# Performance work log

Hardware: AMD Instinct MI355X
Metric: run time of the kernel (lower is better)

The kernel has to match this reference:

```python
import jax, jax.numpy as jnp
import numpy as np

H = W = 2048
TANH_C = 1.1486328125  # probability-correction constant from the model
DEG2RAD = np.float32(np.pi / 180.0)

# Fire-spread direction angle (degrees, East=0, counterclockwise) from the
# neighbor at 3x3 window position (r, c) toward the center cell.
DIR_DEG = jnp.array([[315., 270., 225.],
                     [  0.,   0., 180.],
                     [ 45.,  90., 135.]], dtype=jnp.float32)
CENTER_MASK = jnp.ones((3, 3), jnp.float32).at[1, 1].set(0.0)  # exclude self


def _neighborhood(x):
    """x: [H,W] -> [H,W,3,3] with [i,j,r,c] = x[i+r-1, j+c-1], zero padded."""
    xp = jnp.pad(x, 1)
    return jnp.stack(
        [jnp.stack([xp[r:r + H, c:c + W] for c in range(3)], axis=-1)
         for r in range(3)], axis=-2)


def setup_inputs() -> dict:
    key = jax.random.key(0)
    ks = jax.random.split(key, 8)
    p_veg = jax.random.uniform(ks[0], (H, W), jnp.float32)
    p_den = jax.random.uniform(ks[1], (H, W), jnp.float32)
    wind_velocity = jax.random.uniform(ks[2], (H, W), jnp.float32) * 10.0
    wind_towards_direction = jax.random.uniform(ks[3], (H, W), jnp.float32) * 360.0
    slope = (jax.random.uniform(ks[4], (H, W, 3, 3), jnp.float32) - 0.5) * 60.0
    burning = jax.random.uniform(ks[5], (H, W)) < 0.01  # sparse initial ignition
    burned = jnp.zeros((H, W), dtype=bool)
    rand_ignite = jax.random.uniform(ks[6], (H, W), jnp.float32)
    rand_continue = jax.random.uniform(ks[7], (H, W), jnp.float32)
    return dict(
        p_veg=p_veg, p_den=p_den,
        wind_velocity=wind_velocity, wind_towards_direction=wind_towards_direction,
        slope=slope,
        a=jnp.float32(0.1), p_h=jnp.float32(0.3),
        c_1=jnp.float32(0.1), c_2=jnp.float32(0.1), p_continue=jnp.float32(0.3),
        rand_ignite=rand_ignite, rand_continue=rand_continue,
        burning=burning, burned=burned,
    )


def reference(p_veg, p_den, wind_velocity, wind_towards_direction, slope,
              a, p_h, c_1, c_2, p_continue,
              rand_ignite, rand_continue, burning, burned):
    # p_w = exp(c1*V) * exp(c2*V*(cos(theta_w)-1)), theta_w = angle between
    # wind direction and per-neighbor spread direction. [H,W,3,3]
    theta_w = (wind_towards_direction[..., None, None] - DIR_DEG) * DEG2RAD
    p_w = (jnp.exp(c_1 * wind_velocity)[..., None, None]
           * jnp.exp(c_2 * wind_velocity[..., None, None] * (jnp.cos(theta_w) - 1.0)))
    # p_s = exp(a * theta_s), slope angle in radians. [H,W,3,3]
    p_s = jnp.exp(a * slope * DEG2RAD)
    # p_propagate = tanh(c * p_h*(1+p_veg)*(1+p_den)*p_w*p_s)
    p_base = p_h * (1.0 + p_veg) * (1.0 + p_den)  # [H,W]
    p_prop = jnp.tanh(TANH_C * (p_base[..., None, None] * p_w * p_s))
    # 8-neighbor burning indicators (center masked out). [H,W,3,3]
    nbr_burning = _neighborhood(burning.astype(jnp.float32)) * CENTER_MASK
    # p_ignite = 1 - prod_j (1 - p_propagate_j * burning_j)
    p_ignite = 1.0 - jnp.prod(1.0 - p_prop * nbr_burning, axis=(-2, -1))
    # Stochastic state transition.
    burnable = ~burning & ~burned
    new_ignited = burnable & (rand_ignite < p_ignite)
    keep = burning & (rand_continue < p_continue)
    new_burning = new_ignited | keep
    new_burned = burned | (burning & ~keep)
    return p_ignite, jnp.stack([new_burning, new_burned])
```

## Files before the change

kernel.cpp:

```cpp
#include <hip/hip_runtime.h>
#include <math.h>

namespace {

constexpr int H = 2048;
constexpr int W = 2048;
constexpr int HW = H * W;
constexpr float TANH_C  = 1.1486328125f;
constexpr float DEG2RAD = 0.017453292519943295f;
constexpr float RT2H    = 0.70710678118654752f;
constexpr float LOG2E   = 1.4426950408889634f;
constexpr float TWOPI   = 6.283185307179586f;

__device__ __forceinline__ float fexp2(float x) {
#if __has_builtin(__builtin_amdgcn_exp2f)
    return __builtin_amdgcn_exp2f(x);
#else
    return __exp2f(x);
#endif
}
__device__ __forceinline__ float fcos_rev(float x) {
#if __has_builtin(__builtin_amdgcn_cosf)
    return __builtin_amdgcn_cosf(x);
#else
    return __cosf(x * TWOPI);
#endif
}
__device__ __forceinline__ float fsin_rev(float x) {
#if __has_builtin(__builtin_amdgcn_sinf)
    return __builtin_amdgcn_sinf(x);
#else
    return __sinf(x * TWOPI);
#endif
}
__device__ __forceinline__ float frcp(float x) {
#if __has_builtin(__builtin_amdgcn_rcpf)
    return __builtin_amdgcn_rcpf(x);
#else
    return 1.0f / x;
#endif
}

__global__ __launch_bounds__(256) void wildfire_dense(
    const float* __restrict__ rand_co,
    const int* __restrict__ burning, const int* __restrict__ burned,
    const float* __restrict__ s_pc,
    float* __restrict__ out)
{
    const int idx = ((int)blockIdx.x * 256 + (int)threadIdx.x) * 4;
    const int4   b4  = *reinterpret_cast<const int4*>(burning + idx);
    const int4   bd4 = *reinterpret_cast<const int4*>(burned + idx);
    const float4 rc4 = *reinterpret_cast<const float4*>(rand_co + idx);
    const float  p_cont = s_pc[0];

    const int   bn[4] = {b4.x, b4.y, b4.z, b4.w};
    const int   bd[4] = {bd4.x, bd4.y, bd4.z, bd4.w};
    const float rc[4] = {rc4.x, rc4.y, rc4.z, rc4.w};

    float4 o1, o2;
    float* o1p = &o1.x; float* o2p = &o2.x;
#pragma unroll
    for (int x = 0; x < 4; ++x) {
        const bool isb  = (bn[x] != 0);
        const bool keep = isb && (rc[x] < p_cont);
        o1p[x] = keep ? 1.f : 0.f;
        o2p[x] = ((bd[x] != 0) || (isb && !keep)) ? 1.f : 0.f;
    }
    *reinterpret_cast<float4*>(out + idx)          = make_float4(0.f, 0.f, 0.f, 0.f);
    *reinterpret_cast<float4*>(out + HW + idx)     = o1;
    *reinterpret_cast<float4*>(out + 2 * HW + idx) = o2;
}

__global__ __launch_bounds__(256) void wildfire_heavy(
    const float* __restrict__ p_veg,  const float* __restrict__ p_den,
    const float* __restrict__ wind_v, const float* __restrict__ wind_d,
    const float* __restrict__ slope,
    const float* __restrict__ s_a,  const float* __restrict__ s_ph,
    const float* __restrict__ s_c1, const float* __restrict__ s_c2,
    const float* __restrict__ rand_ig,
    const int* __restrict__ burning, const int* __restrict__ burned,
    float* __restrict__ out)
{
    __shared__ __align__(16) float sb[3][1032];
    __shared__ unsigned short q[1024];
    __shared__ int qn;

    const int t  = (int)threadIdx.x;
    const int i  = (int)blockIdx.y;
    const int j0 = (int)blockIdx.x * 1024;
    const int rowbase = i * W + j0;

    if (t == 0) qn = 0;

    for (int r = 0; r < 3; ++r) {
        const int ii = i + r - 1;
        const bool rowok = (ii >= 0) && (ii < H);
        int4 v = make_int4(0, 0, 0, 0);
        if (rowok)
            v = *reinterpret_cast<const int4*>(burning + ii * W + j0 + 4 * t);
        float4 f;
        f.x = v.x ? 1.f : 0.f;  f.y = v.y ? 1.f : 0.f;
        f.z = v.z ? 1.f : 0.f;  f.w = v.w ? 1.f : 0.f;
        *reinterpret_cast<float4*>(&sb[r][4 + 4 * t]) = f;
        if (t == 0)
            sb[r][3] = (rowok && j0 > 0) ?
                       (burning[ii * W + j0 - 1] ? 1.f : 0.f) : 0.f;
        if (t == 1)
            sb[r][4 + 1024] = (rowok && j0 + 1024 < W) ?
                       (burning[ii * W + j0 + 1024] ? 1.f : 0.f) : 0.f;
    }
    __syncthreads();

    const int jb = t * 4;
    {
        const float4 a = *reinterpret_cast<const float4*>(&sb[0][4 + jb]);
        const float4 b = *reinterpret_cast<const float4*>(&sb[1][4 + jb]);
        const float4 c = *reinterpret_cast<const float4*>(&sb[2][4 + jb]);
        const float r0[6] = {sb[0][3 + jb], a.x, a.y, a.z, a.w, sb[0][8 + jb]};
        const float r1[6] = {sb[1][3 + jb], b.x, b.y, b.z, b.w, sb[1][8 + jb]};
        const float r2[6] = {sb[2][3 + jb], c.x, c.y, c.z, c.w, sb[2][8 + jb]};
#pragma unroll
        for (int x = 0; x < 4; ++x) {
            const float anyn = ((r0[x] + r0[x+1]) + (r0[x+2] + r1[x]))
                             + ((r1[x+2] + r2[x]) + (r2[x+1] + r2[x+2]));
            if (anyn != 0.f) {
                const int pos = atomicAdd(&qn, 1);
                q[pos] = (unsigned short)(jb + x);
            }
        }
    }
    __syncthreads();

    const int n = qn;
    const float a_  = s_a[0];
    const float p_h = s_ph[0];
    const float c1  = s_c1[0];
    const float c2  = s_c2[0];
    const float aslL = (a_ * DEG2RAD) * LOG2E;

    for (int k = t; k < n; k += 256) {
        const int cell = (int)q[k];
        const int c    = 4 + cell;
        const int gidx = rowbase + cell;

        const float pv  = p_veg[gidx];
        const float pd  = p_den[gidx];
        const float wv  = wind_v[gidx];
        const float wd  = wind_d[gidx];
        const float rig = rand_ig[gidx];
        const int   bn  = burned[gidx];
        float sl[9];
        __builtin_memcpy(sl, slope + (size_t)gidx * 9, 9 * sizeof(float));

        const float b0 = sb[0][c-1], b1 = sb[0][c], b2 = sb[0][c+1];
        const float b3 = sb[1][c-1], bcn = sb[1][c], b5 = sb[1][c+1];
        const float b6 = sb[2][c-1], b7 = sb[2][c], b8 = sb[2][c+1];
        const float cnt = ((b0 + b1) + (b2 + b3)) + ((b5 + b6) + (b7 + b8));

        const float wrev = wd * (1.f / 360.f);
        const float cw = fcos_rev(wrev);
        const float sw = fsin_rev(wrev);

        const float Lc2wv = (LOG2E * c2) * wv;
        const float cwv = Lc2wv * cw, swv = Lc2wv * sw;
        const float cwr = RT2H * cwv, swr = RT2H * swv;
        const float dpl = cwr + swr;
        const float dmi = cwr - swr;
        const float p_base = (p_h * (1.f + pv)) * (1.f + pd);
        const float Cz2 = (2.f * LOG2E * TANH_C) * p_base
                        * fexp2(LOG2E * (c1 * wv - c2 * wv));

#define NEIGHBOR(K, b, T, sv)                                            \
        const float q##K = fmaf(aslL, (sv), (T));                        \
        const float z##K = Cz2 * fexp2(q##K);                            \
        const float E##K = fexp2(z##K);                                  \
        const float d##K = fmaf((b), E##K, 1.f);

        NEIGHBOR(0, b0,  dmi, sl[0])
        NEIGHBOR(1, b1, -swv, sl[1])
        NEIGHBOR(2, b2, -dpl, sl[2])
        NEIGHBOR(3, b3,  cwv, sl[3])
        NEIGHBOR(5, b5, -cwv, sl[5])
        NEIGHBOR(6, b6,  dpl, sl[6])
        NEIGHBOR(7, b7,  swv, sl[7])
        NEIGHBOR(8, b8, -dmi, sl[8])
#undef NEIGHBOR
        const float den = ((d0 * d1) * (d2 * d3)) * ((d5 * d6) * (d7 * d8));
        const float num = fexp2(cnt);
        const float pig = fmaf(-num, frcp(den), 1.f);

        out[gidx] = pig;
        const bool ni = (bcn == 0.f) && (bn == 0) && (rig < pig);
        if (ni) out[HW + gidx] = 1.f;
    }
}

}

extern "C" void kernel_launch(void* const* d_in, const int* in_sizes, int n_in,
                              void* d_out, int out_size, void* d_ws, size_t ws_size,
                              hipStream_t stream)
{
    (void)in_sizes; (void)n_in; (void)out_size; (void)d_ws; (void)ws_size;

    {
        dim3 grid(HW / 1024, 1, 1);
        dim3 block(256, 1, 1);
        hipLaunchKernelGGL(wildfire_dense, grid, block, 0, stream,
            (const float*)d_in[11],
            (const int*)d_in[12],
            (const int*)d_in[13],
            (const float*)d_in[9],
            (float*)d_out);
    }
    {
        dim3 grid(W / 1024, H, 1);
        dim3 block(256, 1, 1);
        hipLaunchKernelGGL(wildfire_heavy, grid, block, 0, stream,
            (const float*)d_in[0],  (const float*)d_in[1],
            (const float*)d_in[2],  (const float*)d_in[3],
            (const float*)d_in[4],
            (const float*)d_in[5],  (const float*)d_in[6],
            (const float*)d_in[7],  (const float*)d_in[8],
            (const float*)d_in[10],
            (const int*)d_in[12],   (const int*)d_in[13],
            (float*)d_out);
    }
}
```

Measured before the change: 311.3 us.

## Fuse dense state-transition pass into tiled 2D heavy kernel

Merges the separate dense kernel (zeroing p_ignite, computing keep/burned) into the sparse heavy kernel, so burning is read once into shared memory and reused for both. Switches from one-row blocks to 8x512 tiles, which cuts halo row reloads from three per row to about 1.25, and interleaves tile rows across blockIdx.y. It also reads rand_continue only for 4-cell groups that contain a burning cell. In exchange it adds one launch-free but larger block with more shared memory and a longer serial phase per block before the sparse work.

```diff
diff --git a/kernel.cpp b/kernel.cpp
--- a/kernel.cpp
+++ b/kernel.cpp
@@ -6,6 +6,12 @@
 constexpr int H = 2048;
 constexpr int W = 2048;
 constexpr int HW = H * W;
+constexpr int TR = 8;
+constexpr int TC = 512;
+constexpr int NTX = W / TC;
+constexpr int NTY = H / TR;
+constexpr int BPY = NTY / 8;
+
 constexpr float TANH_C  = 1.1486328125f;
 constexpr float DEG2RAD = 0.017453292519943295f;
 constexpr float RT2H    = 0.70710678118654752f;
@@ -41,93 +47,98 @@
 #endif
 }
 
-__global__ __launch_bounds__(256) void wildfire_dense(
-    const float* __restrict__ rand_co,
-    const int* __restrict__ burning, const int* __restrict__ burned,
-    const float* __restrict__ s_pc,
-    float* __restrict__ out)
-{
-    const int idx = ((int)blockIdx.x * 256 + (int)threadIdx.x) * 4;
-    const int4   b4  = *reinterpret_cast<const int4*>(burning + idx);
-    const int4   bd4 = *reinterpret_cast<const int4*>(burned + idx);
-    const float4 rc4 = *reinterpret_cast<const float4*>(rand_co + idx);
-    const float  p_cont = s_pc[0];
-
-    const int   bn[4] = {b4.x, b4.y, b4.z, b4.w};
-    const int   bd[4] = {bd4.x, bd4.y, bd4.z, bd4.w};
-    const float rc[4] = {rc4.x, rc4.y, rc4.z, rc4.w};
-
-    float4 o1, o2;
-    float* o1p = &o1.x; float* o2p = &o2.x;
-#pragma unroll
-    for (int x = 0; x < 4; ++x) {
-        const bool isb  = (bn[x] != 0);
-        const bool keep = isb && (rc[x] < p_cont);
-        o1p[x] = keep ? 1.f : 0.f;
-        o2p[x] = ((bd[x] != 0) || (isb && !keep)) ? 1.f : 0.f;
-    }
-    *reinterpret_cast<float4*>(out + idx)          = make_float4(0.f, 0.f, 0.f, 0.f);
-    *reinterpret_cast<float4*>(out + HW + idx)     = o1;
-    *reinterpret_cast<float4*>(out + 2 * HW + idx) = o2;
-}
-
-__global__ __launch_bounds__(256) void wildfire_heavy(
+__global__ __launch_bounds__(256) void wildfire_step(
     const float* __restrict__ p_veg,  const float* __restrict__ p_den,
     const float* __restrict__ wind_v, const float* __restrict__ wind_d,
     const float* __restrict__ slope,
     const float* __restrict__ s_a,  const float* __restrict__ s_ph,
     const float* __restrict__ s_c1, const float* __restrict__ s_c2,
-    const float* __restrict__ rand_ig,
+    const float* __restrict__ s_pc,
+    const float* __restrict__ rand_ig, const float* __restrict__ rand_co,
     const int* __restrict__ burning, const int* __restrict__ burned,
     float* __restrict__ out)
 {
-    __shared__ __align__(16) float sb[3][1032];
-    __shared__ unsigned short q[1024];
+    __shared__ __align__(16) float sb[TR + 2][520];
+    __shared__ unsigned short q[TR * TC];
     __shared__ int qn;
 
-    const int t  = (int)threadIdx.x;
-    const int i  = (int)blockIdx.y;
-    const int j0 = (int)blockIdx.x * 1024;
-    const int rowbase = i * W + j0;
+    const int t = (int)threadIdx.x;
+    const int g  = (int)blockIdx.y;
+    const int ty = (g & 7) * BPY + (g >> 3);
+    const int tx = (int)blockIdx.x;
+    const int i0 = ty * TR;
+    const int j0 = tx * TC;
 
     if (t == 0) qn = 0;
 
-    for (int r = 0; r < 3; ++r) {
-        const int ii = i + r - 1;
-        const bool rowok = (ii >= 0) && (ii < H);
+    for (int p = t; p < (TR + 2) * (TC / 4); p += 256) {
+        const int r  = p >> 7;
+        const int gq = p & 127;
+        const int ii = i0 - 1 + r;
         int4 v = make_int4(0, 0, 0, 0);
-        if (rowok)
-            v = *reinterpret_cast<const int4*>(burning + ii * W + j0 + 4 * t);
+        if (ii >= 0 && ii < H)
+            v = *reinterpret_cast<const int4*>(burning + ii * W + j0 + 4 * gq);
         float4 f;
         f.x = v.x ? 1.f : 0.f;  f.y = v.y ? 1.f : 0.f;
         f.z = v.z ? 1.f : 0.f;  f.w = v.w ? 1.f : 0.f;
-        *reinterpret_cast<float4*>(&sb[r][4 + 4 * t]) = f;
-        if (t == 0)
-            sb[r][3] = (rowok && j0 > 0) ?
-                       (burning[ii * W + j0 - 1] ? 1.f : 0.f) : 0.f;
-        if (t == 1)
-            sb[r][4 + 1024] = (rowok && j0 + 1024 < W) ?
-                       (burning[ii * W + j0 + 1024] ? 1.f : 0.f) : 0.f;
+        *reinterpret_cast<float4*>(&sb[r][4 + 4 * gq]) = f;
+    }
+    if (t < TR + 2) {
+        const int ii = i0 - 1 + t;
+        sb[t][3] = (ii >= 0 && ii < H && j0 > 0)
+                 ? (burning[ii * W + j0 - 1] ? 1.f : 0.f) : 0.f;
+    } else if (t >= 64 && t < 64 + TR + 2) {
+        const int r  = t - 64;
+        const int ii = i0 - 1 + r;
+        sb[r][4 + TC] = (ii >= 0 && ii < H && j0 + TC < W)
+                 ? (burning[ii * W + j0 + TC] ? 1.f : 0.f) : 0.f;
     }
     __syncthreads();
 
-    const int jb = t * 4;
-    {
-        const float4 a = *reinterpret_cast<const float4*>(&sb[0][4 + jb]);
-        const float4 b = *reinterpret_cast<const float4*>(&sb[1][4 + jb]);
-        const float4 c = *reinterpret_cast<const float4*>(&sb[2][4 + jb]);
-        const float r0[6] = {sb[0][3 + jb], a.x, a.y, a.z, a.w, sb[0][8 + jb]};
-        const float r1[6] = {sb[1][3 + jb], b.x, b.y, b.z, b.w, sb[1][8 + jb]};
-        const float r2[6] = {sb[2][3 + jb], c.x, c.y, c.z, c.w, sb[2][8 + jb]};
+    const float p_cont = s_pc[0];
+#pragma unroll
+    for (int k = 0; k < 4; ++k) {
+        const int p   = t + (k << 8);
+        const int row = p >> 7;
+        const int jb  = (p & 127) * 4;
+        const float4 a = *reinterpret_cast<const float4*>(&sb[row][4 + jb]);
+        const float4 b = *reinterpret_cast<const float4*>(&sb[row + 1][4 + jb]);
+        const float4 c = *reinterpret_cast<const float4*>(&sb[row + 2][4 + jb]);
+        const float r0[6] = {sb[row][3 + jb],     a.x, a.y, a.z, a.w, sb[row][8 + jb]};
+        const float r1[6] = {sb[row + 1][3 + jb], b.x, b.y, b.z, b.w, sb[row + 1][8 + jb]};
+        const float r2[6] = {sb[row + 2][3 + jb], c.x, c.y, c.z, c.w, sb[row + 2][8 + jb]};
+
+        bool isb[4];
 #pragma unroll
         for (int x = 0; x < 4; ++x) {
             const float anyn = ((r0[x] + r0[x+1]) + (r0[x+2] + r1[x]))
                              + ((r1[x+2] + r2[x]) + (r2[x+1] + r2[x+2]));
+            isb[x] = (r1[x+1] != 0.f);
             if (anyn != 0.f) {
                 const int pos = atomicAdd(&qn, 1);
-                q[pos] = (unsigned short)(jb + x);
+                q[pos] = (unsigned short)(row * TC + jb + x);
             }
         }
+
+        const int gidx = (i0 + row) * W + j0 + jb;
+        const int4 bd4 = *reinterpret_cast<const int4*>(burned + gidx);
+        const int  bn[4] = {bd4.x, bd4.y, bd4.z, bd4.w};
+        float rc[4] = {1.f, 1.f, 1.f, 1.f};
+        if (isb[0] || isb[1] || isb[2] || isb[3]) {
+            const float4 v = *reinterpret_cast<const float4*>(rand_co + gidx);
+            rc[0] = v.x; rc[1] = v.y; rc[2] = v.z; rc[3] = v.w;
+        }
+        float4 o1, o2;
+        float* o1p = &o1.x; float* o2p = &o2.x;
+#pragma unroll
+        for (int x = 0; x < 4; ++x) {
+            const bool keep = isb[x] && (rc[x] < p_cont);
+            o1p[x] = keep ? 1.f : 0.f;
+            o2p[x] = ((bn[x] != 0) || (isb[x] && !keep)) ? 1.f : 0.f;
+        }
+        *reinterpret_cast<float4*>(out + gidx)          = make_float4(0.f, 0.f, 0.f, 0.f);
+        *reinterpret_cast<float4*>(out + HW + gidx)     = o1;
+        *reinterpret_cast<float4*>(out + 2 * HW + gidx) = o2;
     }
     __syncthreads();
 
@@ -140,8 +151,9 @@
 
     for (int k = t; k < n; k += 256) {
         const int cell = (int)q[k];
-        const int c    = 4 + cell;
-        const int gidx = rowbase + cell;
+        const int row  = cell >> 9;
+        const int col  = cell & 511;
+        const int gidx = (i0 + row) * W + j0 + col;
 
         const float pv  = p_veg[gidx];
         const float pd  = p_den[gidx];
@@ -152,9 +164,9 @@
         float sl[9];
         __builtin_memcpy(sl, slope + (size_t)gidx * 9, 9 * sizeof(float));
 
-        const float b0 = sb[0][c-1], b1 = sb[0][c], b2 = sb[0][c+1];
-        const float b3 = sb[1][c-1], bcn = sb[1][c], b5 = sb[1][c+1];
-        const float b6 = sb[2][c-1], b7 = sb[2][c], b8 = sb[2][c+1];
+        const float b0 = sb[row][3+col],   b1 = sb[row][4+col],    b2 = sb[row][5+col];
+        const float b3 = sb[row+1][3+col], bcn = sb[row+1][4+col], b5 = sb[row+1][5+col];
+        const float b6 = sb[row+2][3+col], b7 = sb[row+2][4+col],  b8 = sb[row+2][5+col];
         const float cnt = ((b0 + b1) + (b2 + b3)) + ((b5 + b6) + (b7 + b8));
 
         const float wrev = wd * (1.f / 360.f);
@@ -202,28 +214,16 @@
                               hipStream_t stream)
 {
     (void)in_sizes; (void)n_in; (void)out_size; (void)d_ws; (void)ws_size;
-
-    {
-        dim3 grid(HW / 1024, 1, 1);
-        dim3 block(256, 1, 1);
-        hipLaunchKernelGGL(wildfire_dense, grid, block, 0, stream,
-            (const float*)d_in[11],
-            (const int*)d_in[12],
-            (const int*)d_in[13],
-            (const float*)d_in[9],
-            (float*)d_out);
-    }
-    {
-        dim3 grid(W / 1024, H, 1);
-        dim3 block(256, 1, 1);
-        hipLaunchKernelGGL(wildfire_heavy, grid, block, 0, stream,
-            (const float*)d_in[0],  (const float*)d_in[1],
-            (const float*)d_in[2],  (const float*)d_in[3],
-            (const float*)d_in[4],
-            (const float*)d_in[5],  (const float*)d_in[6],
-            (const float*)d_in[7],  (const float*)d_in[8],
-            (const float*)d_in[10],
-            (const int*)d_in[12],   (const int*)d_in[13],
-            (float*)d_out);
-    }
-}
+    dim3 grid(NTX, NTY, 1);
+    dim3 block(256, 1, 1);
+    hipLaunchKernelGGL(wildfire_step, grid, block, 0, stream,
+        (const float*)d_in[0],  (const float*)d_in[1],
+        (const float*)d_in[2],  (const float*)d_in[3],
+        (const float*)d_in[4],
+        (const float*)d_in[5],  (const float*)d_in[6],
+        (const float*)d_in[7],  (const float*)d_in[8],
+        (const float*)d_in[9],
+        (const float*)d_in[10], (const float*)d_in[11],
+        (const int*)d_in[12],   (const int*)d_in[13],
+        (float*)d_out);
+}
```

After: 305.9 us. Within noise of the previous version (-1.7%).
